# Optimization experiments

Hardware: AMD Instinct MI355X
Metric: run time of the kernel (lower is better)

The kernel has to match this reference:

```python
import jax, jax.numpy as jnp
import numpy as np

B = 32
HIST, C, H, W = 10, 11, 15, 20
D, NH, NL = 256, 4, 4
HD = D // NH
OUT, ADIM = 256, 20
L = HIST * H * W + 1  # 3001 tokens incl. cls
VIS = HIST * C * H * W  # 33000


def layernorm(x, g, b, eps=1e-5):
    m = jnp.mean(x, axis=-1, keepdims=True)
    v = jnp.mean((x - m) ** 2, axis=-1, keepdims=True)
    return (x - m) * jax.lax.rsqrt(v + eps) * g + b


def rope_1d(x):
    # x: [B, NH, L, HD]
    l, hd = x.shape[2], x.shape[3]
    t = jnp.arange(l, dtype=x.dtype)
    freqs = 10000.0 ** (-jnp.arange(0, hd, 2, dtype=x.dtype) / hd)
    emb = t[:, None] * freqs[None, :]            # [L, HD/2]
    emb = jnp.concatenate([emb, emb], axis=-1)   # [L, HD]
    cos = jnp.cos(emb)[None, None]
    sin = jnp.sin(emb)[None, None]
    x1, x2 = x[..., : hd // 2], x[..., hd // 2 :]
    rot = jnp.concatenate([-x2, x1], axis=-1)
    return x * cos + rot * sin


def lightning_attn(x, qw, kw, vw, ow, gq, bq, gk, bk):
    b, l, _ = x.shape
    q = layernorm(x @ qw, gq, bq)
    k = layernorm(x @ kw, gk, bk)
    v = x @ vw
    split = lambda a: a.reshape(b, l, NH, HD).transpose(0, 2, 1, 3)  # [B,NH,L,HD]
    q, k, v = split(q), split(k), split(v)
    q = jax.nn.silu(rope_1d(q))
    k = jax.nn.silu(rope_1d(k))
    kv = jnp.einsum('bhld,bhle->bhde', k, v)            # O(L) kv accumulation
    out = jnp.einsum('bhld,bhde->bhle', q, kv)
    out = out / jnp.sqrt(jnp.asarray(HD, x.dtype))
    out = out.transpose(0, 2, 1, 3).reshape(b, l, D)
    return out @ ow


def forward(obs_stack, proj_w, proj_b, cls_token, qw, kw, vw, ow, gq, bq, gk, bk,
            n1g, n1b, n2g, n2b, w1, b1, w2, b2, fng, fnb, out_w, out_b):
    b = obs_stack.shape[0]
    obs_feat = obs_stack[:, :VIS]
    action_feat = obs_stack[:, VIS:]
    vision = obs_feat.reshape(b, HIST, C, H, W).transpose(0, 1, 3, 4, 2)  # [B,T,H,W,C]
    x = vision @ proj_w + proj_b                                          # [B,T,H,W,D]
    x = x.reshape(b, -1, D)
    cls = jnp.broadcast_to(cls_token, (b, 1, D))
    x = jnp.concatenate([cls, x], axis=1)                                 # [B,L,D]
    for i in range(NL):
        h = lightning_attn(layernorm(x, n1g[i], n1b[i]), qw[i], kw[i], vw[i], ow[i],
                           gq[i], bq[i], gk[i], bk[i])
        x = x + h
        y = layernorm(x, n2g[i], n2b[i])
        y = jax.nn.gelu(y @ w1[i] + b1[i], approximate=False) @ w2[i] + b2[i]
        x = x + y
    x = layernorm(x, fng, fnb)
    cls_out = x[:, 0, :]
    final = jnp.concatenate([cls_out, action_feat], axis=1)
    return final @ out_w + out_b


def setup_inputs() -> dict:
    key = jax.random.key(0)
    ks = jax.random.split(key, 16)
    s = 0.02
    n = lambda k, shp: jax.random.normal(k, shp, dtype=jnp.float32) * s
    inp = {
        'obs_stack': jax.random.normal(ks[0], (B, VIS + ADIM), dtype=jnp.float32),
        'proj_w': n(ks[1], (C, D)),
        'proj_b': jnp.zeros((D,), jnp.float32),
        'cls_token': jax.random.normal(ks[2], (1, 1, D), dtype=jnp.float32),
        'qw': n(ks[3], (NL, D, D)),
        'kw': n(ks[4], (NL, D, D)),
        'vw': n(ks[5], (NL, D, D)),
        'ow': n(ks[6], (NL, D, D)),
        'gq': jnp.ones((NL, D), jnp.float32),
        'bq': jnp.zeros((NL, D), jnp.float32),
        'gk': jnp.ones((NL, D), jnp.float32),
        'bk': jnp.zeros((NL, D), jnp.float32),
        'n1g': jnp.ones((NL, D), jnp.float32),
        'n1b': jnp.zeros((NL, D), jnp.float32),
        'n2g': jnp.ones((NL, D), jnp.float32),
        'n2b': jnp.zeros((NL, D), jnp.float32),
        'w1': n(ks[7], (NL, D, 4 * D)),
        'b1': jnp.zeros((NL, 4 * D), jnp.float32),
        'w2': n(ks[8], (NL, 4 * D, D)),
        'b2': jnp.zeros((NL, D), jnp.float32),
        'fng': jnp.ones((D,), jnp.float32),
        'fnb': jnp.zeros((D,), jnp.float32),
        'out_w': n(ks[9], (D + ADIM, OUT)),
        'out_b': jnp.zeros((OUT,), jnp.float32),
    }
    return inp


def reference(obs_stack, proj_w, proj_b, cls_token, qw, kw, vw, ow, gq, bq, gk, bk,
              n1g, n1b, n2g, n2b, w1, b1, w2, b2, fng, fnb, out_w, out_b):
    return forward(obs_stack, proj_w, proj_b, cls_token, qw, kw, vw, ow, gq, bq, gk, bk,
                   n1g, n1b, n2g, n2b, w1, b1, w2, b2, fng, fnb, out_w, out_b)
```

## Files before the change

### kernel.cpp

```cpp
#include <hip/hip_runtime.h>
#include <math.h>

typedef unsigned short u16;
typedef __attribute__((ext_vector_type(8))) short short8;
typedef __attribute__((ext_vector_type(4))) short short4v;
typedef __attribute__((ext_vector_type(4))) float f32x4;

constexpr int B_    = 32;
constexpr int HIST_ = 10, C_ = 11, H_ = 15, W_ = 20;
constexpr int D_    = 256, NH_ = 4, NL_ = 4, HD_ = 64;
constexpr int OUT_  = 256, ADIM_ = 20;
constexpr int L_    = HIST_*H_*W_ + 1;
constexpr int VIS_  = HIST_*C_*H_*W_;
constexpr int NTOK  = B_*L_;
constexpr int OBSROW = VIS_ + ADIM_;
constexpr int PADR  = 128;

__device__ __forceinline__ float bf2f(u16 u) {
    return __uint_as_float(((unsigned)u) << 16);
}
__device__ __forceinline__ u16 f2bf(float f) {
    unsigned u = __float_as_uint(f);
    u = u + 0x7FFFu + ((u >> 16) & 1u);
    return (u16)(u >> 16);
}
__device__ __forceinline__ f32x4 mfma16(short8 a, short8 b, f32x4 c) {
    return __builtin_amdgcn_mfma_f32_16x16x32_bf16(a, b, c, 0, 0, 0);
}
__device__ __forceinline__ void gload16(const u16* gsrc, u16* ldsdst) {
    __builtin_amdgcn_global_load_lds(
        (const __attribute__((address_space(1))) unsigned int*)gsrc,
        (__attribute__((address_space(3))) unsigned int*)ldsdst,
        16, 0, 0);
}
__device__ __forceinline__ float gelu_fast(float v) {
    float t2 = 1.5957691216f*(v + 0.044715f*v*v*v);
    return v / (1.f + __expf(-t2));
}

__global__ void zero_kernel(float* __restrict__ p, int n) {
    int i = blockIdx.x*256 + threadIdx.x;
    if (i < n) p[i] = 0.f;
}

__global__ void wcvt_kernel(const float* __restrict__ src, u16* __restrict__ dst,
                            int Nn, int Kk, int dstLS, int dstOff) {
    int idx = blockIdx.x*256 + threadIdx.x;
    int tot = NL_*Nn*Kk;
    if (idx >= tot) return;
    int l = idx / (Nn*Kk);
    int rem = idx % (Nn*Kk);
    int n = rem / Kk, k = rem % Kk;
    dst[(size_t)l*dstLS + (size_t)(dstOff+n)*Kk + k] = f2bf(src[(size_t)l*Kk*Nn + (size_t)k*Nn + n]);
}

__global__ void rope_table_kernel(float* __restrict__ tab) {
    int idx = blockIdx.x*256 + threadIdx.x;
    if (idx >= L_*32) return;
    int t = idx >> 5, i = idx & 31;
    float freq = powf(10000.f, -2.f*(float)i/(float)HD_);
    float ang = (float)t * freq;
    tab[idx*2]   = cosf(ang);
    tab[idx*2+1] = sinf(ang);
}

__global__ __launch_bounds__(256) void proj_kernel(const float* __restrict__ obs,
        const float* __restrict__ pw, const float* __restrict__ pb,
        const float* __restrict__ cls, float* __restrict__ x) {
    int wave = threadIdx.x >> 6, lane = threadIdx.x & 63;
    int n = blockIdx.x*4 + wave;
    if (n >= NTOK) return;
    int b = n / L_, l = n % L_;
    float4 acc;
    if (l == 0) {
        acc = ((const float4*)cls)[lane];
    } else {
        int t = l - 1;
        int hist = t / (H_*W_);
        int rem  = t % (H_*W_);
        float vv = 0.f;
        if (lane < C_) vv = obs[(size_t)b*OBSROW + hist*(C_*H_*W_) + lane*(H_*W_) + rem];
        acc = ((const float4*)pb)[lane];
        #pragma unroll
        for (int c = 0; c < C_; ++c) {
            float vc = __shfl(vv, c);
            float4 w4 = ((const float4*)(pw + c*D_))[lane];
            acc.x += vc*w4.x; acc.y += vc*w4.y; acc.z += vc*w4.z; acc.w += vc*w4.w;
        }
    }
    ((float4*)(x + (size_t)n*D_))[lane] = acc;
}

__global__ __launch_bounds__(256) void ln_f2b_kernel(const float* __restrict__ in,
        const float* __restrict__ g, const float* __restrict__ bt,
        u16* __restrict__ out, int ntok) {
    int wave = threadIdx.x >> 6, lane = threadIdx.x & 63;
    int n = blockIdx.x*4 + wave;
    if (n >= ntok) return;
    float4 v = ((const float4*)(in + (size_t)n*D_))[lane];
    float s  = v.x + v.y + v.z + v.w;
    float sq = v.x*v.x + v.y*v.y + v.z*v.z + v.w*v.w;
    #pragma unroll
    for (int off = 32; off; off >>= 1) { s += __shfl_xor(s, off); sq += __shfl_xor(sq, off); }
    float mean = s * (1.f/D_);
    float var  = sq * (1.f/D_) - mean*mean;
    float r = rsqrtf(var + 1e-5f);
    float4 gg = ((const float4*)g)[lane];
    float4 bb = ((const float4*)bt)[lane];
    short4v o;
    o.x = (short)f2bf((v.x-mean)*r*gg.x + bb.x);
    o.y = (short)f2bf((v.y-mean)*r*gg.y + bb.y);
    o.z = (short)f2bf((v.z-mean)*r*gg.z + bb.z);
    o.w = (short)f2bf((v.w-mean)*r*gg.w + bb.w);
    *(short4v*)(out + (size_t)n*D_ + lane*4) = o;
}

__global__ __launch_bounds__(256) void lnres_kernel(float* __restrict__ x,
        u16* __restrict__ dx, const float* __restrict__ g, const float* __restrict__ bt,
        int ntok) {
    int wave = threadIdx.x >> 6, lane = threadIdx.x & 63;
    int n = blockIdx.x*4 + wave;
    if (n >= ntok) return;
    float4 v = ((const float4*)(x + (size_t)n*D_))[lane];
    short4v d = *(const short4v*)(dx + (size_t)n*D_ + lane*4);
    v.x += bf2f((u16)d.x); v.y += bf2f((u16)d.y);
    v.z += bf2f((u16)d.z); v.w += bf2f((u16)d.w);
    ((float4*)(x + (size_t)n*D_))[lane] = v;
    float s  = v.x + v.y + v.z + v.w;
    float sq = v.x*v.x + v.y*v.y + v.z*v.z + v.w*v.w;
    #pragma unroll
    for (int off = 32; off; off >>= 1) { s += __shfl_xor(s, off); sq += __shfl_xor(sq, off); }
    float mean = s * (1.f/D_);
    float var  = sq * (1.f/D_) - mean*mean;
    float r = rsqrtf(var + 1e-5f);
    float4 gg = ((const float4*)g)[lane];
    float4 bb = ((const float4*)bt)[lane];
    short4v o;
    o.x = (short)f2bf((v.x-mean)*r*gg.x + bb.x);
    o.y = (short)f2bf((v.y-mean)*r*gg.y + bb.y);
    o.z = (short)f2bf((v.z-mean)*r*gg.z + bb.z);
    o.w = (short)f2bf((v.w-mean)*r*gg.w + bb.w);
    *(short4v*)(dx + (size_t)n*D_ + lane*4) = o;
}

__global__ __launch_bounds__(256) void lnrope_kernel(u16* __restrict__ q,
        const float* __restrict__ g, const float* __restrict__ bt,
        const float* __restrict__ tab, int ntok, int ld) {
    int wave = threadIdx.x >> 6, lane = threadIdx.x & 63;
    int n = blockIdx.x*4 + wave;
    if (n >= ntok) return;
    int l = n % L_;
    short4v raw = *(const short4v*)(q + (size_t)n*ld + lane*4);
    float v0 = bf2f((u16)raw.x), v1 = bf2f((u16)raw.y), v2 = bf2f((u16)raw.z), v3 = bf2f((u16)raw.w);
    float s  = v0+v1+v2+v3;
    float sq = v0*v0+v1*v1+v2*v2+v3*v3;
    #pragma unroll
    for (int off = 32; off; off >>= 1) { s += __shfl_xor(s, off); sq += __shfl_xor(sq, off); }
    float mean = s * (1.f/D_);
    float var  = sq * (1.f/D_) - mean*mean;
    float r = rsqrtf(var + 1e-5f);
    float4 gg = ((const float4*)g)[lane];
    float4 bb = ((const float4*)bt)[lane];
    float o0 = (v0-mean)*r*gg.x + bb.x;
    float o1 = (v1-mean)*r*gg.y + bb.y;
    float o2 = (v2-mean)*r*gg.z + bb.z;
    float o3 = (v3-mean)*r*gg.w + bb.w;
    float p0 = __shfl_xor(o0, 8), p1 = __shfl_xor(o1, 8);
    float p2 = __shfl_xor(o2, 8), p3 = __shfl_xor(o3, 8);
    bool first = (lane & 15) < 8;
    const float4* tp = (const float4*)(tab + ((size_t)l*32 + (lane&7)*4)*2);
    float4 t01 = tp[0], t23 = tp[1];
    float r0 = first ? o0*t01.x - p0*t01.y : o0*t01.x + p0*t01.y;
    float r1 = first ? o1*t01.z - p1*t01.w : o1*t01.z + p1*t01.w;
    float r2 = first ? o2*t23.x - p2*t23.y : o2*t23.x + p2*t23.y;
    float r3 = first ? o3*t23.z - p3*t23.w : o3*t23.z + p3*t23.w;
    r0 = r0 / (1.f + expf(-r0));
    r1 = r1 / (1.f + expf(-r1));
    r2 = r2 / (1.f + expf(-r2));
    r3 = r3 / (1.f + expf(-r3));
    short4v o;
    o.x = (short)f2bf(r0); o.y = (short)f2bf(r1);
    o.z = (short)f2bf(r2); o.w = (short)f2bf(r3);
    *(short4v*)(q + (size_t)n*ld + lane*4) = o;
}

template<int EPI, bool PB>
__global__ __launch_bounds__(256) void gemm_bf16(const u16* __restrict__ A, int lda,
        const u16* __restrict__ Wt, const float* __restrict__ bias,
        u16* __restrict__ Cb, float* __restrict__ Xres, int M, int N, int K, int ldc) {
    __shared__ u16 As[2*128*32];
    __shared__ u16 Bs[2*128*32];
    const int gx = gridDim.x;
    int n = blockIdx.y * gx + blockIdx.x;
    const int nwg = gx * gridDim.y;
    if ((nwg & 7) == 0) n = (n & 7) * (nwg >> 3) + (n >> 3);
    const int bx = n % gx, by = n / gx;
    const int row0 = by*128, col0 = bx*128;

    size_t zrow = 0;
    if (PB) {
        int z = blockIdx.z;
        A  += (size_t)z * M * lda;
        Wt += (size_t)z * N * K;
        zrow = (size_t)z * M;
    }

    const int tid = threadIdx.x;
    const int wid = tid >> 6, lane = tid & 63;
    const int wr = wid >> 1, wc = wid & 1;

    f32x4 acc[4][4];
    #pragma unroll
    for (int i = 0; i < 4; ++i)
        #pragma unroll
        for (int j = 0; j < 4; ++j) {
            f32x4 z; z.x = 0.f; z.y = 0.f; z.z = 0.f; z.w = 0.f;
            acc[i][j] = z;
        }

    const int r0s = wid*32 + (lane>>2);
    const int r1s = r0s + 16;
    const int s0 = ((lane&3) - (r0s>>1)) & 3;
    const int s1 = ((lane&3) - (r1s>>1)) & 3;
    const u16* a0p = A  + (size_t)(row0 + r0s)*lda + s0*8;
    const u16* a1p = A  + (size_t)(row0 + r1s)*lda + s1*8;
    const u16* b0p = Wt + (size_t)(col0 + r0s)*K + s0*8;
    const u16* b1p = Wt + (size_t)(col0 + r1s)*K + s1*8;
    u16* lA0 = As + (wid*2+0)*512;
    u16* lA1 = As + (wid*2+1)*512;
    u16* lB0 = Bs + (wid*2+0)*512;
    u16* lB1 = Bs + (wid*2+1)*512;

    const int kg = lane >> 4, li = lane & 15;
    int aoff[4], boff[4];
    #pragma unroll
    for (int mi = 0; mi < 4; ++mi) {
        int row = wr*64 + mi*16 + li;
        aoff[mi] = row*32 + ((kg + (row>>1)) & 3)*8;
    }
    #pragma unroll
    for (int ni = 0; ni < 4; ++ni) {
        int row = wc*64 + ni*16 + li;
        boff[ni] = row*32 + ((kg + (row>>1)) & 3)*8;
    }

    auto stage = [&](int k0) {
        #pragma unroll
        for (int t = 0; t < 2; ++t) {
            const int ko = k0 + t*32;
            const int lo = t*4096;
            gload16(a0p + ko, lA0 + lo); gload16(a1p + ko, lA1 + lo);
            gload16(b0p + ko, lB0 + lo); gload16(b1p + ko, lB1 + lo);
        }
    };

    stage(0);
    const int nk2 = K >> 6;
    for (int ks = 0; ks < nk2; ++ks) {
        __syncthreads();
        short8 af[2][4], bfr[2][4];
        #pragma unroll
        for (int t = 0; t < 2; ++t) {
            #pragma unroll
            for (int mi = 0; mi < 4; ++mi) af[t][mi] = *(const short8*)(As + t*4096 + aoff[mi]);
            #pragma unroll
            for (int ni = 0; ni < 4; ++ni) bfr[t][ni] = *(const short8*)(Bs + t*4096 + boff[ni]);
        }
        __syncthreads();
        if (ks + 1 < nk2) stage((ks + 1) << 6);
        #pragma unroll
        for (int t = 0; t < 2; ++t)
            #pragma unroll
            for (int mi = 0; mi < 4; ++mi)
                #pragma unroll
                for (int ni = 0; ni < 4; ++ni)
                    acc[mi][ni] = mfma16(af[t][mi], bfr[t][ni], acc[mi][ni]);
    }

    #pragma unroll
    for (int mi = 0; mi < 4; ++mi) {
        int rbase = row0 + wr*64 + mi*16 + kg*4;
        #pragma unroll
        for (int ni = 0; ni < 4; ++ni) {
            int col = col0 + wc*64 + ni*16 + li;
            #pragma unroll
            for (int r = 0; r < 4; ++r) {
                int row = rbase + r;
                if (row >= M) continue;
                float v = acc[mi][ni][r];
                if (EPI == 1 || EPI == 3 || EPI == 4) v += bias[col];
                if (EPI == 1) v = gelu_fast(v);
                if (EPI == 0 || EPI == 1 || EPI == 4)
                    Cb[(zrow + row)*(size_t)ldc + col] = f2bf(v);
                else
                    Xres[(zrow + row)*(size_t)ldc + col] += v;
            }
        }
    }
}

template<int EPI, bool PB>
__global__ __launch_bounds__(512) void gemm_wide(const u16* __restrict__ A, int lda,
        const u16* __restrict__ Wt, const float* __restrict__ bias,
        u16* __restrict__ Cb, int M, int N, int K, int ldc) {
    __shared__ u16 As[2*4096];
    __shared__ u16 Bs[2*8192];
    const int gx = gridDim.x;
    int n = blockIdx.y * gx + blockIdx.x;
    const int nwg = gx * gridDim.y;
    if ((nwg & 7) == 0) n = (n & 7) * (nwg >> 3) + (n >> 3);
    const int bx = n % gx, by = n / gx;
    const int row0 = by*128, col0 = bx*256;

    size_t zrow = 0;
    if (PB) {
        int z = blockIdx.z;
        A  += (size_t)z * M * lda;
        Wt += (size_t)z * N * K;
        zrow = (size_t)z * M;
    }

    const int tid = threadIdx.x;
    const int wid = tid >> 6, lane = tid & 63;
    const int kg = lane >> 4, li = lane & 15;

    f32x4 acc[16];
    #pragma unroll
    for (int i = 0; i < 16; ++i) { f32x4 z; z.x=0.f; z.y=0.f; z.z=0.f; z.w=0.f; acc[i]=z; }

    const int ra = wid*16 + (lane>>2);
    const int sa = ((lane&3) - (ra>>1)) & 3;
    const u16* agp = A + (size_t)(row0 + ra)*lda + sa*8;
    const int lAo = wid*512;
    const int rb0 = (wid*2+0)*16 + (lane>>2);
    const int rb1 = (wid*2+1)*16 + (lane>>2);
    const int sb0 = ((lane&3) - (rb0>>1)) & 3;
    const int sb1 = ((lane&3) - (rb1>>1)) & 3;
    const u16* bgp0 = Wt + (size_t)(col0 + rb0)*K + sb0*8;
    const u16* bgp1 = Wt + (size_t)(col0 + rb1)*K + sb1*8;
    const int lB0o = (wid*2+0)*512;
    const int lB1o = (wid*2+1)*512;

    const int arow = wid*16 + li;
    const int aoff = arow*32 + ((kg + (arow>>1)) & 3)*8;
    int boff[16];
    #pragma unroll
    for (int ni = 0; ni < 16; ++ni) {
        int row = ni*16 + li;
        boff[ni] = row*32 + ((kg + (row>>1)) & 3)*8;
    }

    auto stage = [&](int k0) {
        #pragma unroll
        for (int t = 0; t < 2; ++t) {
            const int ko = k0 + t*32;
            gload16(agp  + ko, As + t*4096 + lAo);
            gload16(bgp0 + ko, Bs + t*8192 + lB0o);
            gload16(bgp1 + ko, Bs + t*8192 + lB1o);
        }
    };

    stage(0);
    const int nk2 = K >> 6;
    for (int ks = 0; ks < nk2; ++ks) {
        __syncthreads();
        short8 af0 = *(const short8*)(As + aoff);
        short8 b0[8], b1[8];
        #pragma unroll
        for (int ni = 0; ni < 8; ++ni) b0[ni] = *(const short8*)(Bs + boff[ni]);
        #pragma unroll
        for (int ni = 0; ni < 8; ++ni) acc[ni] = mfma16(af0, b0[ni], acc[ni]);
        #pragma unroll
        for (int ni = 0; ni < 8; ++ni) b1[ni] = *(const short8*)(Bs + boff[8+ni]);
        #pragma unroll
        for (int ni = 0; ni < 8; ++ni) acc[8+ni] = mfma16(af0, b1[ni], acc[8+ni]);
        short8 af1 = *(const short8*)(As + 4096 + aoff);
        #pragma unroll
        for (int ni = 0; ni < 8; ++ni) b0[ni] = *(const short8*)(Bs + 8192 + boff[ni]);
        #pragma unroll
        for (int ni = 0; ni < 8; ++ni) b1[ni] = *(const short8*)(Bs + 8192 + boff[8+ni]);
        __syncthreads();
        if (ks + 1 < nk2) stage((ks + 1) << 6);
        #pragma unroll
        for (int ni = 0; ni < 8; ++ni) acc[ni]   = mfma16(af1, b0[ni], acc[ni]);
        #pragma unroll
        for (int ni = 0; ni < 8; ++ni) acc[8+ni] = mfma16(af1, b1[ni], acc[8+ni]);
    }

    #pragma unroll
    for (int r = 0; r < 4; ++r) {
        const int row = row0 + wid*16 + kg*4 + r;
        if (row >= M) continue;
        #pragma unroll
        for (int ni = 0; ni < 16; ++ni) {
            int col = col0 + ni*16 + li;
            float v = acc[ni][r];
            if (EPI == 1 || EPI == 2) v += bias[col];
            if (EPI == 1) v = gelu_fast(v);
            Cb[(zrow + row)*(size_t)ldc + col] = f2bf(v);
        }
    }
}

constexpr int KV_LSPLIT = 4;
constexpr int KV_PART   = 768;
__global__ __launch_bounds__(256) void kv_mfma_kernel(const u16* __restrict__ Kt,
        const u16* __restrict__ Vt, float* __restrict__ kvf, int ld) {
    __shared__ u16 kT[64][34];
    __shared__ u16 vT[64][34];
    const int bh = blockIdx.x;
    const int b = bh >> 2, h = bh & 3;
    const int tid = threadIdx.x;
    const int wid = tid >> 6, lane = tid & 63;
    const int kg = lane >> 4, li = lane & 15;
    const int wm = (wid >> 1)*32, wn = (wid & 1)*32;
    const int sl = tid >> 3;
    const int sd = (tid & 7) * 8;
    const u16* kbase = Kt + ((size_t)b*L_)*ld + h*HD_ + sd;
    const u16* vbase = Vt + ((size_t)b*L_)*ld + h*HD_ + sd;

    f32x4 acc[2][2];
    #pragma unroll
    for (int i = 0; i < 2; ++i)
        #pragma unroll
        for (int j = 0; j < 2; ++j) {
            f32x4 z; z.x=0.f; z.y=0.f; z.z=0.f; z.w=0.f; acc[i][j] = z;
        }

    const int l0p = blockIdx.y * KV_PART;
    for (int t = 0; t < KV_PART/32; ++t) {
        int gl = l0p + t*32 + sl;
        short8 kk = {0,0,0,0,0,0,0,0}, vv = {0,0,0,0,0,0,0,0};
        if (gl < L_) {
            kk = *(const short8*)(kbase + (size_t)gl*ld);
            vv = *(const short8*)(vbase + (size_t)gl*ld);
        }
        __syncthreads();
        #pragma unroll
        for (int j = 0; j < 8; ++j) {
            kT[sd+j][sl] = (u16)kk[j];
            vT[sd+j][sl] = (u16)vv[j];
        }
        __syncthreads();
        short8 a0, a1, b0, b1;
        {
            uint* d0 = (uint*)&a0; const uint* p0 = (const uint*)&kT[wm + li][kg*8];
            uint* d1 = (uint*)&a1; const uint* p1 = (const uint*)&kT[wm + 16 + li][kg*8];
            uint* d2 = (uint*)&b0; const uint* p2 = (const uint*)&vT[wn + li][kg*8];
            uint* d3 = (uint*)&b1; const uint* p3 = (const uint*)&vT[wn + 16 + li][kg*8];
            #pragma unroll
            for (int j = 0; j < 4; ++j) { d0[j]=p0[j]; d1[j]=p1[j]; d2[j]=p2[j]; d3[j]=p3[j]; }
        }
        acc[0][0] = mfma16(a0, b0, acc[0][0]);
        acc[0][1] = mfma16(a0, b1, acc[0][1]);
        acc[1][0] = mfma16(a1, b0, acc[1][0]);
        acc[1][1] = mfma16(a1, b1, acc[1][1]);
    }
    float* base = kvf + (size_t)bh*4096;
    #pragma unroll
    for (int mi = 0; mi < 2; ++mi)
        #pragma unroll
        for (int ni = 0; ni < 2; ++ni)
            #pragma unroll
            for (int r = 0; r < 4; ++r)
                atomicAdd(base + (wm + mi*16 + kg*4 + r)*64 + wn + ni*16 + li,
                          acc[mi][ni][r]);
}

__global__ __launch_bounds__(256) void m2_kernel(const float* __restrict__ kvf,
        const float* __restrict__ ow, u16* __restrict__ m2t) {
    __shared__ float kvs[64][64];
    const int bh = blockIdx.x;
    const int b = bh >> 2, h = bh & 3;
    const int tid = threadIdx.x;
    #pragma unroll
    for (int p = 0; p < 16; ++p)
        ((float*)kvs)[p*256 + tid] = kvf[(size_t)bh*4096 + p*256 + tid];
    __syncthreads();
    float acc[64];
    #pragma unroll
    for (int d = 0; d < 64; ++d) acc[d] = 0.f;
    for (int e = 0; e < 64; ++e) {
        float w = ow[(size_t)(h*64 + e)*256 + tid];
        #pragma unroll
        for (int d = 0; d < 64; ++d) acc[d] += kvs[d][e] * w;
    }
    u16* dst = m2t + ((size_t)b*256 + tid)*256 + h*64;
    #pragma unroll
    for (int d = 0; d < 64; ++d) dst[d] = f2bf(acc[d]*0.125f);
}

__global__ void head_kernel(const float* __restrict__ x, const float* __restrict__ obs,
                            const float* __restrict__ fng, const float* __restrict__ fnb,
                            const float* __restrict__ ow, const float* __restrict__ ob,
                            float* __restrict__ out) {
    __shared__ float row[D_ + ADIM_];
    __shared__ float red[8];
    int b = blockIdx.x, tid = threadIdx.x;
    float v = x[((size_t)b*L_)*D_ + tid];
    float s = v, sq = v*v;
    #pragma unroll
    for (int off = 32; off; off >>= 1) { s += __shfl_xor(s, off); sq += __shfl_xor(sq, off); }
    int wave = tid >> 6, lane = tid & 63;
    if (lane == 0) { red[wave] = s; red[4+wave] = sq; }
    __syncthreads();
    s  = red[0]+red[1]+red[2]+red[3];
    sq = red[4]+red[5]+red[6]+red[7];
    float mean = s*(1.f/D_), var = sq*(1.f/D_) - mean*mean;
    float r = rsqrtf(var + 1e-5f);
    row[tid] = (v-mean)*r*fng[tid] + fnb[tid];
    if (tid < ADIM_) row[D_+tid] = obs[(size_t)b*OBSROW + VIS_ + tid];
    __syncthreads();
    float acc = ob[tid];
    for (int j = 0; j < D_+ADIM_; ++j) acc += row[j]*ow[j*OUT_ + tid];
    out[(size_t)b*OUT_ + tid] = acc;
}

extern "C" void kernel_launch(void* const* d_in, const int* in_sizes, int n_in,
                              void* d_out, int out_size, void* d_ws, size_t ws_size,
                              hipStream_t stream) {
    const float* obs   = (const float*)d_in[0];
    const float* pw    = (const float*)d_in[1];
    const float* pb    = (const float*)d_in[2];
    const float* cls   = (const float*)d_in[3];
    const float* qw    = (const float*)d_in[4];
    const float* kw    = (const float*)d_in[5];
    const float* vw    = (const float*)d_in[6];
    const float* oww   = (const float*)d_in[7];
    const float* gq    = (const float*)d_in[8];
    const float* bq    = (const float*)d_in[9];
    const float* gk    = (const float*)d_in[10];
    const float* bk    = (const float*)d_in[11];
    const float* n1g   = (const float*)d_in[12];
    const float* n1b   = (const float*)d_in[13];
    const float* n2g   = (const float*)d_in[14];
    const float* n2b   = (const float*)d_in[15];
    const float* w1    = (const float*)d_in[16];
    const float* b1    = (const float*)d_in[17];
    const float* w2    = (const float*)d_in[18];
    const float* b2    = (const float*)d_in[19];
    const float* fng   = (const float*)d_in[20];
    const float* fnb   = (const float*)d_in[21];
    const float* outw  = (const float*)d_in[22];
    const float* outb  = (const float*)d_in[23];

    float* x = (float*)d_ws;
    u16* qkvT = (u16*)(x + (size_t)NTOK*D_);
    u16* w1T  = qkvT + (size_t)NL_*768*256;
    u16* w2T  = w1T  + (size_t)NL_*262144;
    float* tab = (float*)(w2T + (size_t)NL_*262144);
    u16* bufs = (u16*)(tab + (size_t)L_*32*2);

    size_t fixedB = (size_t)((char*)bufs - (char*)d_ws);
    auto needed = [&](int nb) -> size_t {
        size_t t = (size_t)nb * L_;
        return fixedB + (t*256 + (size_t)PADR*256)*2 + (t*1024 + (size_t)PADR*1024)*2
               + (size_t)nb*65536*2 + (size_t)nb*NH_*4096*4;
    };
    int nbc = 32;
    while (nbc > 1 && needed(nbc) > ws_size) nbc >>= 1;
    const int nch = B_ / nbc;
    const int RCn = nbc * L_;

    u16* Xn   = bufs;
    u16* QKVc = Xn + (size_t)RCn*256 + (size_t)PADR*256;
    u16* Hc   = QKVc;
    u16* M2T  = QKVc + (size_t)RCn*1024 + (size_t)PADR*1024;
    float* kvf = (float*)(M2T + (size_t)nbc*65536);

    wcvt_kernel<<<(NL_*65536 + 255)/256, 256, 0, stream>>>(qw,  qkvT, 256, 256, 768*256, 0);
    wcvt_kernel<<<(NL_*65536 + 255)/256, 256, 0, stream>>>(kw,  qkvT, 256, 256, 768*256, 256);
    wcvt_kernel<<<(NL_*65536 + 255)/256, 256, 0, stream>>>(vw,  qkvT, 256, 256, 768*256, 512);
    wcvt_kernel<<<(NL_*262144 + 255)/256, 256, 0, stream>>>(w1, w1T, 1024, 256, 262144, 0);
    wcvt_kernel<<<(NL_*262144 + 255)/256, 256, 0, stream>>>(w2, w2T, 256, 1024, 262144, 0);
    rope_table_kernel<<<(L_*32 + 255)/256, 256, 0, stream>>>(tab);
    proj_kernel<<<(NTOK + 3)/4, 256, 0, stream>>>(obs, pw, pb, cls, x);

    const int gy  = (RCn + 127)/128;
    const int lnb = (RCn + 3)/4;
    const int nbh = nbc*NH_;

    for (int c = 0; c < nch; ++c) {
        float* xc = x + (size_t)c*RCn*D_;
        ln_f2b_kernel<<<lnb, 256, 0, stream>>>(xc, n1g, n1b, Xn, RCn);

        for (int layer = 0; layer < NL_; ++layer) {
            const u16* qkvT_l = qkvT + (size_t)layer*768*256;
            const u16* w1T_l  = w1T  + (size_t)layer*262144;
            const u16* w2T_l  = w2T  + (size_t)layer*262144;
            const float* ow_l = oww + (size_t)layer*65536;
            const float* b1_l = b1 + (size_t)layer*1024;
            const float* b2_l = b2 + (size_t)layer*D_;

            gemm_wide<0,false><<<dim3(3, gy), 512, 0, stream>>>(Xn, 256, qkvT_l, nullptr, QKVc, RCn, 768, 256, 768);
            lnrope_kernel<<<lnb, 256, 0, stream>>>(QKVc,       gq + layer*D_, bq + layer*D_, tab, RCn, 768);
            lnrope_kernel<<<lnb, 256, 0, stream>>>(QKVc + 256, gk + layer*D_, bk + layer*D_, tab, RCn, 768);
            zero_kernel<<<(nbh*4096 + 255)/256, 256, 0, stream>>>(kvf, nbh*4096);
            kv_mfma_kernel<<<dim3(nbh, KV_LSPLIT), 256, 0, stream>>>(QKVc + 256, QKVc + 512, kvf, 768);
            m2_kernel<<<nbh, 256, 0, stream>>>(kvf, ow_l, M2T);
            gemm_bf16<0,true><<<dim3(2, 24, nbc), 256, 0, stream>>>(QKVc, 768, M2T, nullptr, Xn, nullptr, L_, 256, 256, 256);
            lnres_kernel<<<lnb, 256, 0, stream>>>(xc, Xn, n2g + layer*D_, n2b + layer*D_, RCn);
            gemm_wide<1,false><<<dim3(4, gy), 512, 0, stream>>>(Xn, 256, w1T_l, b1_l, Hc, RCn, 1024, 256, 1024);
            gemm_bf16<4,false><<<dim3(2, gy), 256, 0, stream>>>(Hc, 1024, w2T_l, b2_l, Xn, nullptr, RCn, 256, 1024, 256);
            const float* gN = (layer < NL_-1) ? (n1g + (layer+1)*D_) : fng;
            const float* bN = (layer < NL_-1) ? (n1b + (layer+1)*D_) : fnb;
            lnres_kernel<<<lnb, 256, 0, stream>>>(xc, Xn, gN, bN, RCn);
        }
    }

    head_kernel<<<B_, 256, 0, stream>>>(x, obs, fng, fnb, outw, outb, (float*)d_out);
}
```

Before: 2.526 ms.

## Fuse residual add and LayerNorm into full-width output GEMM epilogues

```diff
diff --git a/kernel.cpp b/kernel.cpp
--- a/kernel.cpp
+++ b/kernel.cpp
@@ -113,34 +113,6 @@
     o.z = (short)f2bf((v.z-mean)*r*gg.z + bb.z);
     o.w = (short)f2bf((v.w-mean)*r*gg.w + bb.w);
     *(short4v*)(out + (size_t)n*D_ + lane*4) = o;
-}
-
-__global__ __launch_bounds__(256) void lnres_kernel(float* __restrict__ x,
-        u16* __restrict__ dx, const float* __restrict__ g, const float* __restrict__ bt,
-        int ntok) {
-    int wave = threadIdx.x >> 6, lane = threadIdx.x & 63;
-    int n = blockIdx.x*4 + wave;
-    if (n >= ntok) return;
-    float4 v = ((const float4*)(x + (size_t)n*D_))[lane];
-    short4v d = *(const short4v*)(dx + (size_t)n*D_ + lane*4);
-    v.x += bf2f((u16)d.x); v.y += bf2f((u16)d.y);
-    v.z += bf2f((u16)d.z); v.w += bf2f((u16)d.w);
-    ((float4*)(x + (size_t)n*D_))[lane] = v;
-    float s  = v.x + v.y + v.z + v.w;
-    float sq = v.x*v.x + v.y*v.y + v.z*v.z + v.w*v.w;
-    #pragma unroll
-    for (int off = 32; off; off >>= 1) { s += __shfl_xor(s, off); sq += __shfl_xor(sq, off); }
-    float mean = s * (1.f/D_);
-    float var  = sq * (1.f/D_) - mean*mean;
-    float r = rsqrtf(var + 1e-5f);
-    float4 gg = ((const float4*)g)[lane];
-    float4 bb = ((const float4*)bt)[lane];
-    short4v o;
-    o.x = (short)f2bf((v.x-mean)*r*gg.x + bb.x);
-    o.y = (short)f2bf((v.y-mean)*r*gg.y + bb.y);
-    o.z = (short)f2bf((v.z-mean)*r*gg.z + bb.z);
-    o.w = (short)f2bf((v.w-mean)*r*gg.w + bb.w);
-    *(short4v*)(dx + (size_t)n*D_ + lane*4) = o;
 }
 
 __global__ __launch_bounds__(256) void lnrope_kernel(u16* __restrict__ q,
@@ -288,12 +260,9 @@
                 int row = rbase + r;
                 if (row >= M) continue;
                 float v = acc[mi][ni][r];
-                if (EPI == 1 || EPI == 3 || EPI == 4) v += bias[col];
+                if (EPI == 1 || EPI == 4) v += bias[col];
                 if (EPI == 1) v = gelu_fast(v);
-                if (EPI == 0 || EPI == 1 || EPI == 4)
-                    Cb[(zrow + row)*(size_t)ldc + col] = f2bf(v);
-                else
-                    Xres[(zrow + row)*(size_t)ldc + col] += v;
+                Cb[(zrow + row)*(size_t)ldc + col] = f2bf(v);
             }
         }
     }
@@ -395,9 +364,133 @@
         for (int ni = 0; ni < 16; ++ni) {
             int col = col0 + ni*16 + li;
             float v = acc[ni][r];
-            if (EPI == 1 || EPI == 2) v += bias[col];
-            if (EPI == 1) v = gelu_fast(v);
+            if (EPI == 1) { v += bias[col]; v = gelu_fast(v); }
             Cb[(zrow + row)*(size_t)ldc + col] = f2bf(v);
+        }
+    }
+}
+
+template<int EPI, bool PB>
+__global__ __launch_bounds__(256) void gemm_w64(const u16* __restrict__ A, int lda,
+        const u16* __restrict__ Wt, const float* __restrict__ bias,
+        float* __restrict__ Xres, u16* __restrict__ Xn,
+        const float* __restrict__ g, const float* __restrict__ bt,
+        int M, int K) {
+    __shared__ u16 As[2*2048];
+    __shared__ u16 Bs[2*8192];
+    const int by = blockIdx.y;
+    const int row0 = by*64, col0 = 0;
+
+    size_t zrow = 0;
+    if (PB) {
+        int z = blockIdx.z;
+        A  += (size_t)z * M * lda;
+        Wt += (size_t)z * 256 * K;
+        zrow = (size_t)z * M;
+    }
+
+    const int tid = threadIdx.x;
+    const int wid = tid >> 6, lane = tid & 63;
+    const int kg = lane >> 4, li = lane & 15;
+
+    f32x4 acc[16];
+    #pragma unroll
+    for (int i = 0; i < 16; ++i) { f32x4 z; z.x=0.f; z.y=0.f; z.z=0.f; z.w=0.f; acc[i]=z; }
+
+    const int ra = wid*16 + (lane>>2);
+    const int sa = ((lane&3) - (ra>>1)) & 3;
+    const u16* agp = A + (size_t)(row0 + ra)*lda + sa*8;
+    const int lAo = wid*512;
+    const u16* bgp[4];
+    int lBo[4];
+    #pragma unroll
+    for (int i = 0; i < 4; ++i) {
+        int rb = (wid*4+i)*16 + (lane>>2);
+        int sb = ((lane&3) - (rb>>1)) & 3;
+        bgp[i] = Wt + (size_t)(col0 + rb)*K + sb*8;
+        lBo[i] = (wid*4+i)*512;
+    }
+
+    const int arow = wid*16 + li;
+    const int aoff = arow*32 + ((kg + (arow>>1)) & 3)*8;
+    int boff[16];
+    #pragma unroll
+    for (int ni = 0; ni < 16; ++ni) {
+        int row = ni*16 + li;
+        boff[ni] = row*32 + ((kg + (row>>1)) & 3)*8;
+    }
+
+    auto stage = [&](int k0) {
+        #pragma unroll
+        for (int t = 0; t < 2; ++t) {
+            const int ko = k0 + t*32;
+            gload16(agp + ko, As + t*2048 + lAo);
+            #pragma unroll
+            for (int i = 0; i < 4; ++i)
+                gload16(bgp[i] + ko, Bs + t*8192 + lBo[i]);
+        }
+    };
+
+    stage(0);
+    const int nk2 = K >> 6;
+    for (int ks = 0; ks < nk2; ++ks) {
+        __syncthreads();
+        short8 af0 = *(const short8*)(As + aoff);
+        short8 b0[8], b1[8];
+        #pragma unroll
+        for (int ni = 0; ni < 8; ++ni) b0[ni] = *(const short8*)(Bs + boff[ni]);
+        #pragma unroll
+        for (int ni = 0; ni < 8; ++ni) acc[ni] = mfma16(af0, b0[ni], acc[ni]);
+        #pragma unroll
+        for (int ni = 0; ni < 8; ++ni) b1[ni] = *(const short8*)(Bs + boff[8+ni]);
+        #pragma unroll
+        for (int ni = 0; ni < 8; ++ni) acc[8+ni] = mfma16(af0, b1[ni], acc[8+ni]);
+        short8 af1 = *(const short8*)(As + 2048 + aoff);
+        #pragma unroll
+        for (int ni = 0; ni < 8; ++ni) b0[ni] = *(const short8*)(Bs + 8192 + boff[ni]);
+        #pragma unroll
+        for (int ni = 0; ni < 8; ++ni) b1[ni] = *(const short8*)(Bs + 8192 + boff[8+ni]);
+        __syncthreads();
+        if (ks + 1 < nk2) stage((ks + 1) << 6);
+        #pragma unroll
+        for (int ni = 0; ni < 8; ++ni) acc[ni]   = mfma16(af1, b0[ni], acc[ni]);
+        #pragma unroll
+        for (int ni = 0; ni < 8; ++ni) acc[8+ni] = mfma16(af1, b1[ni], acc[8+ni]);
+    }
+
+    #pragma unroll
+    for (int r = 0; r < 4; ++r) {
+        const int row = row0 + wid*16 + kg*4 + r;
+        const bool ok = row < M;
+        float vv[16];
+        float s = 0.f, sq = 0.f;
+        #pragma unroll
+        for (int ni = 0; ni < 16; ++ni) {
+            int col = ni*16 + li;
+            float v = acc[ni][r];
+            if (EPI == 6) v += bias[col];
+            if (ok) {
+                size_t xi = (zrow + row)*(size_t)256 + col;
+                v += Xres[xi];
+                Xres[xi] = v;
+            }
+            vv[ni] = v;
+            s += v; sq += v*v;
+        }
+        s += __shfl_xor(s, 1); sq += __shfl_xor(sq, 1);
+        s += __shfl_xor(s, 2); sq += __shfl_xor(sq, 2);
+        s += __shfl_xor(s, 4); sq += __shfl_xor(sq, 4);
+        s += __shfl_xor(s, 8); sq += __shfl_xor(sq, 8);
+        float mean = s * (1.f/256.f);
+        float var  = sq * (1.f/256.f) - mean*mean;
+        float rstd = rsqrtf(var + 1e-5f);
+        if (ok) {
+            #pragma unroll
+            for (int ni = 0; ni < 16; ++ni) {
+                int col = ni*16 + li;
+                float xn = (vv[ni] - mean)*rstd*g[col] + bt[col];
+                Xn[(zrow + row)*(size_t)256 + col] = f2bf(xn);
+            }
         }
     }
 }
@@ -577,6 +670,8 @@
     proj_kernel<<<(NTOK + 3)/4, 256, 0, stream>>>(obs, pw, pb, cls, x);
 
     const int gy  = (RCn + 127)/128;
+    const int gy64 = (RCn + 63)/64;
+    const int gy64b = (L_ + 63)/64;
     const int lnb = (RCn + 3)/4;
     const int nbh = nbc*NH_;
 
@@ -598,13 +693,11 @@
             zero_kernel<<<(nbh*4096 + 255)/256, 256, 0, stream>>>(kvf, nbh*4096);
             kv_mfma_kernel<<<dim3(nbh, KV_LSPLIT), 256, 0, stream>>>(QKVc + 256, QKVc + 512, kvf, 768);
             m2_kernel<<<nbh, 256, 0, stream>>>(kvf, ow_l, M2T);
-            gemm_bf16<0,true><<<dim3(2, 24, nbc), 256, 0, stream>>>(QKVc, 768, M2T, nullptr, Xn, nullptr, L_, 256, 256, 256);
-            lnres_kernel<<<lnb, 256, 0, stream>>>(xc, Xn, n2g + layer*D_, n2b + layer*D_, RCn);
+            gemm_w64<5,true><<<dim3(1, gy64b, nbc), 256, 0, stream>>>(QKVc, 768, M2T, nullptr, xc, Xn, n2g + layer*D_, n2b + layer*D_, L_, 256);
             gemm_wide<1,false><<<dim3(4, gy), 512, 0, stream>>>(Xn, 256, w1T_l, b1_l, Hc, RCn, 1024, 256, 1024);
-            gemm_bf16<4,false><<<dim3(2, gy), 256, 0, stream>>>(Hc, 1024, w2T_l, b2_l, Xn, nullptr, RCn, 256, 1024, 256);
             const float* gN = (layer < NL_-1) ? (n1g + (layer+1)*D_) : fng;
             const float* bN = (layer < NL_-1) ? (n1b + (layer+1)*D_) : fnb;
-            lnres_kernel<<<lnb, 256, 0, stream>>>(xc, Xn, gN, bN, RCn);
+            gemm_w64<6,false><<<dim3(1, gy64), 256, 0, stream>>>(Hc, 1024, w2T_l, b2_l, xc, Xn, gN, bN, RCn, 1024);
         }
     }
 
```

New measurement: 3.057 ms. 21.0% more time.
